# Performance work log

Hardware: AMD Instinct MI355X
Metric: run time of the kernel (lower is better)

The kernel has to match this reference:

```python
import jax, jax.numpy as jnp
import numpy as np

EPS = 1e-6  # torch.nn.PairwiseDistance default eps: dist = ||x - y + eps||_2


def setup_inputs() -> dict:
    key = jax.random.key(0)
    k1, k2 = jax.random.split(key)
    samples = jax.random.normal(k1, (4096, 128), dtype=jnp.float32)   # batch of observations
    V = jax.random.uniform(k2, (65536, 128), dtype=jnp.float32)       # grown node codebook (torch.rand init)
    return {"samples": samples, "V": V}


def reference(samples, V):
    # activate_bmu, vectorized over the batch.
    # torch PairwiseDistance(p=2): d_n = || x - V_n + eps ||_2
    D = samples.shape[-1]
    x_sq = jnp.sum(samples * samples, axis=-1)        # [B]
    v_sq = jnp.sum(V * V, axis=-1)                    # [N]
    xv = jnp.einsum('bd,nd->bn', samples, V)          # [B, N]
    x_sum = jnp.sum(samples, axis=-1)                 # [B]
    v_sum = jnp.sum(V, axis=-1)                       # [N]
    sq = (x_sq[:, None] + v_sq[None, :] - 2.0 * xv
          + 2.0 * EPS * (x_sum[:, None] - v_sum[None, :]) + D * EPS * EPS)
    dists = jnp.sqrt(jnp.maximum(sq, 0.0))            # [B, N]
    # top-2 smallest distances -> BMU b, second BMU s
    neg_top2, idx = jax.lax.top_k(-dists, 2)          # [B, 2]
    b = idx[:, 0]
    s = idx[:, 1]
    a = jnp.exp(neg_top2[:, 0])                       # exp(-b_dist)
    return (b, s, a)
```

## Files before the change

### kernel.cpp

```cpp
#include <hip/hip_runtime.h>
#include <math.h>

#define NS 4096
#define NV 65536
#define DDIM 128
#define EPSV 1e-6f
#define NCHUNK 16
#define TILES_PER_CHUNK 32
#define FLTMAX 3.402823466e+38f
#define IMAX 0x7fffffff

#define VSQ_F   0
#define VSUM_F  65536
#define XSQ_F   131072
#define XSUM_F  135168
#define PART_F  139264
#define WS_TILED_BYTE 1605632
#define TILE_BYTES 65536
#define TILE_STRIDE 66560

typedef __attribute__((ext_vector_type(8)))  __bf16        bf16x8;
typedef __attribute__((ext_vector_type(8)))  unsigned short ush8;
typedef __attribute__((ext_vector_type(4)))  unsigned short ush4;
typedef __attribute__((ext_vector_type(16))) float          f32x16;

typedef const __attribute__((address_space(1))) unsigned int* gp_t;
typedef __attribute__((address_space(3))) unsigned int*       lp_t;

__device__ __forceinline__ void async_cp16(const void* g, void* l) {
    __builtin_amdgcn_global_load_lds((gp_t)g, (lp_t)l, 16, 0, 0);
}

__device__ __forceinline__ unsigned short f2bf(float x) {
    unsigned u = __builtin_bit_cast(unsigned, x);
    u += 0x7FFFu + ((u >> 16) & 1u);
    return (unsigned short)(u >> 16);
}
__device__ __forceinline__ float bf2f(unsigned short h) {
    unsigned u = ((unsigned)h) << 16;
    return __builtin_bit_cast(float, u);
}

__device__ __forceinline__ void merge2t(float& d1, int& i1, float& d2, int& i2,
                                        float d, int i) {
    bool b1 = (d < d1) || (d == d1 && i < i1);
    bool b2 = (d < d2) || (d == d2 && i < i2);
    if (b1) { d2 = d1; i2 = i1; d1 = d; i1 = i; }
    else if (b2) { d2 = d; i2 = i; }
}

__global__ void vq_precompute(const float* __restrict__ samples,
                              const float* __restrict__ V,
                              float* __restrict__ ws) {
    const int wave = threadIdx.x >> 6;
    const int lane = threadIdx.x & 63;
    int row = blockIdx.x * 4 + wave;
    const float* src; float* sqo; float* sumo; int r;
    if (row < NV) {
        r = row; src = V + (size_t)r * DDIM; sqo = ws + VSQ_F; sumo = ws + VSUM_F;
    } else {
        r = row - NV;
        if (r >= NS) return;
        src = samples + (size_t)r * DDIM; sqo = ws + XSQ_F; sumo = ws + XSUM_F;
    }
    float2 v = ((const float2*)src)[lane];
    float s = v.x + v.y;
    float q = v.x * v.x + v.y * v.y;
    #pragma unroll
    for (int off = 32; off >= 1; off >>= 1) {
        s += __shfl_xor(s, off);
        q += __shfl_xor(q, off);
    }
    if (lane == 0) { sqo[r] = q; sumo[r] = s; }
}

__global__ void vq_cj(const float* __restrict__ ws_f, char* __restrict__ ws) {
    int c = blockIdx.x * 256 + threadIdx.x;
    float cj = ws_f[VSQ_F + c] - 2.0f * EPSV * ws_f[VSUM_F + c];
    int tile = c >> 7, m = c & 127;
    *(float*)(ws + WS_TILED_BYTE + (size_t)tile * TILE_STRIDE + TILE_BYTES + m * 4) = cj;
}

__global__ void vq_convertV(const float* __restrict__ V, char* __restrict__ ws) {
    const int tile = blockIdx.x;
    const int tid = threadIdx.x;
    char* dst = ws + WS_TILED_BYTE + (size_t)tile * TILE_STRIDE;
    const float4* v4 = (const float4*)V;
    #pragma unroll
    for (int i = 0; i < 16; i++) {
        int flat = i * 256 + tid;
        int row = flat >> 5;
        int kq  = flat & 31;
        float4 g = v4[(size_t)(tile * 128 + row) * 32 + kq];
        int k0 = kq * 4;
        int s = k0 >> 4, q = (k0 >> 3) & 1, j0 = k0 & 7;
        float xs[4] = {g.x, g.y, g.z, g.w};
        ush4 h, l;
        #pragma unroll
        for (int e = 0; e < 4; e++) {
            unsigned short hh = f2bf(xs[e]);
            h[e] = hh;
            l[e] = f2bf(xs[e] - bf2f(hh));
        }
        *(ush4*)(dst + ((((s * 2 + 0) * 2 + q) * 128) + row) * 16 + j0 * 2) = h;
        *(ush4*)(dst + ((((s * 2 + 1) * 2 + q) * 128) + row) * 16 + j0 * 2) = l;
    }
}

__global__ __launch_bounds__(256, 2)
void vq_gemm_topk(const float* __restrict__ samples, char* __restrict__ ws) {
    __shared__ __align__(16) char lds[TILE_STRIDE];
    const int tid = threadIdx.x;
    const int w = tid >> 6, lane = tid & 63;
    const int l31 = lane & 31, q = lane >> 5;
    const int st = blockIdx.x;
    const int chunk = blockIdx.y;
    const int nrow = st * 128 + w * 32 + l31;

    ush8 bh[8], bl[8];
    const float4* s4 = (const float4*)samples;
    #pragma unroll
    for (int s = 0; s < 8; s++) {
        float4 x0 = s4[(size_t)nrow * 32 + s * 4 + q * 2];
        float4 x1 = s4[(size_t)nrow * 32 + s * 4 + q * 2 + 1];
        float xs[8] = {x0.x, x0.y, x0.z, x0.w, x1.x, x1.y, x1.z, x1.w};
        #pragma unroll
        for (int j = 0; j < 8; j++) {
            float y = -2.0f * xs[j];
            unsigned short hh = f2bf(y);
            bh[s][j] = hh;
            bl[s][j] = f2bf(y - bf2f(hh));
        }
    }

    float d1 = FLTMAX, d2 = FLTMAX;
    int i1 = IMAX, i2 = IMAX;

    const char* tile0 = ws + WS_TILED_BYTE + (size_t)(chunk * TILES_PER_CHUNK) * TILE_STRIDE;

    for (int it = 0; it < TILES_PER_CHUNK; it++) {
        const char* src = tile0 + (size_t)it * TILE_STRIDE;
        #pragma unroll
        for (int i = 0; i < 16; i++) {
            int off = (i * 256 + tid) * 16;
            async_cp16(src + off, lds + off);
        }
        if (tid < 64) {
            int off = TILE_BYTES + tid * 16;
            async_cp16(src + off, lds + off);
        }
        __syncthreads();

        f32x16 acc[4];
        #pragma unroll
        for (int mi = 0; mi < 4; mi++)
            #pragma unroll
            for (int r = 0; r < 16; r++) acc[mi][r] = 0.0f;

        #pragma unroll
        for (int s = 0; s < 8; s++) {
            bf16x8 bhs = __builtin_bit_cast(bf16x8, bh[s]);
            bf16x8 bls = __builtin_bit_cast(bf16x8, bl[s]);
            #pragma unroll
            for (int mi = 0; mi < 4; mi++) {
                bf16x8 ah = *(const bf16x8*)(lds + (size_t)((((s * 2 + 0) * 2 + q) * 128) + mi * 32 + l31) * 16);
                bf16x8 al = *(const bf16x8*)(lds + (size_t)((((s * 2 + 1) * 2 + q) * 128) + mi * 32 + l31) * 16);
                acc[mi] = __builtin_amdgcn_mfma_f32_32x32x16_bf16(ah, bhs, acc[mi], 0, 0, 0);
                acc[mi] = __builtin_amdgcn_mfma_f32_32x32x16_bf16(ah, bls, acc[mi], 0, 0, 0);
                acc[mi] = __builtin_amdgcn_mfma_f32_32x32x16_bf16(al, bhs, acc[mi], 0, 0, 0);
            }
        }

        const int cbase = chunk * 4096 + it * 128 + 4 * q;
        #pragma unroll
        for (int mi = 0; mi < 4; mi++) {
            #pragma unroll
            for (int g = 0; g < 4; g++) {
                float4 cj = *(const float4*)(lds + TILE_BYTES + (size_t)(mi * 32 + g * 8 + 4 * q) * 4);
                float cje[4] = {cj.x, cj.y, cj.z, cj.w};
                #pragma unroll
                for (int e = 0; e < 4; e++) {
                    float v = acc[mi][g * 4 + e] + cje[e];
                    int idx = cbase + mi * 32 + g * 8 + e;
                    bool c1 = v < d1, c2 = v < d2;
                    float nd2 = c1 ? d1 : v;
                    int   ni2 = c1 ? i1 : idx;
                    d2 = c2 ? nd2 : d2;
                    i2 = c2 ? ni2 : i2;
                    d1 = c1 ? v : d1;
                    i1 = c1 ? idx : i1;
                }
            }
        }
        __syncthreads();
    }

    {
        float od1 = __shfl_xor(d1, 32), od2 = __shfl_xor(d2, 32);
        int   oi1 = __shfl_xor(i1, 32), oi2 = __shfl_xor(i2, 32);
        merge2t(d1, i1, d2, i2, od1, oi1);
        merge2t(d1, i1, d2, i2, od2, oi2);
    }
    if (q == 0) {
        int sample = st * 128 + w * 32 + l31;
        float4* part = (float4*)( (float*)((char*)ws) + PART_F );
        part[(size_t)sample * NCHUNK + chunk] = make_float4(d1, d2, (float)i1, (float)i2);
    }
}

__global__ void vq_reduce(const float* __restrict__ ws_f, float* __restrict__ out) {
    int m = blockIdx.x * 256 + threadIdx.x;
    if (m >= NS) return;
    const float4* part = (const float4*)(ws_f + PART_F);
    float d1 = FLTMAX, d2 = FLTMAX;
    int i1 = IMAX, i2 = IMAX;
    for (int c = 0; c < NCHUNK; c++) {
        float4 p = part[(size_t)m * NCHUNK + c];
        merge2t(d1, i1, d2, i2, p.x, (int)p.z);
        merge2t(d1, i1, d2, i2, p.y, (int)p.w);
    }
    float ci = ws_f[XSQ_F + m] + 2.0f * EPSV * ws_f[XSUM_F + m] + (float)DDIM * EPSV * EPSV;
    float sq = fmaxf(ci + d1, 0.0f);
    out[m]          = (float)i1;
    out[NS + m]     = (float)i2;
    out[2 * NS + m] = expf(-sqrtf(sq));
}

extern "C" void kernel_launch(void* const* d_in, const int* in_sizes, int n_in,
                              void* d_out, int out_size, void* d_ws, size_t ws_size,
                              hipStream_t stream) {
    (void)in_sizes; (void)n_in; (void)out_size; (void)ws_size;
    const float* samples = (const float*)d_in[0];
    const float* V = (const float*)d_in[1];
    float* out = (float*)d_out;
    float* ws_f = (float*)d_ws;
    char*  ws_b = (char*)d_ws;

    vq_precompute<<<dim3((NV + NS) / 4), 256, 0, stream>>>(samples, V, ws_f);
    vq_cj<<<dim3(NV / 256), 256, 0, stream>>>(ws_f, ws_b);
    vq_convertV<<<dim3(NV / 128), 256, 0, stream>>>(V, ws_b);
    vq_gemm_topk<<<dim3(NS / 128, NCHUNK), 256, 0, stream>>>(samples, ws_b);
    vq_reduce<<<dim3(NS / 256), 256, 0, stream>>>(ws_f, out);
}
```

Measured before the change: 299.1 us.

## Double-buffer codebook tiles, widen GEMM block to 512 threads, fuse cj precompute

Fuses the cj computation into the norm precompute kernel, which removes one launch. vq_convertV now writes 16-byte stores per row. The main GEMM kernel uses 512 threads, with each block covering 256 samples split across a 2x4 wave grid. Codebook tiles are double-buffered in LDS with async copies so the next tile loads while the current one is computed. The top-2 update is skipped via a wave ballot when no lane improves, and a final LDS merge combines the two wave rows. The cost is more LDS per block and more registers per wave, which may limit occupancy.

```diff
diff --git a/kernel.cpp b/kernel.cpp
--- a/kernel.cpp
+++ b/kernel.cpp
@@ -10,18 +10,16 @@
 #define FLTMAX 3.402823466e+38f
 #define IMAX 0x7fffffff
 
-#define VSQ_F   0
-#define VSUM_F  65536
 #define XSQ_F   131072
 #define XSUM_F  135168
 #define PART_F  139264
 #define WS_TILED_BYTE 1605632
 #define TILE_BYTES 65536
 #define TILE_STRIDE 66560
+#define BUFB 66560
 
 typedef __attribute__((ext_vector_type(8)))  __bf16        bf16x8;
 typedef __attribute__((ext_vector_type(8)))  unsigned short ush8;
-typedef __attribute__((ext_vector_type(4)))  unsigned short ush4;
 typedef __attribute__((ext_vector_type(16))) float          f32x16;
 
 typedef const __attribute__((address_space(1))) unsigned int* gp_t;
@@ -51,18 +49,15 @@
 
 __global__ void vq_precompute(const float* __restrict__ samples,
                               const float* __restrict__ V,
-                              float* __restrict__ ws) {
+                              float* __restrict__ ws_f, char* __restrict__ ws_b) {
     const int wave = threadIdx.x >> 6;
     const int lane = threadIdx.x & 63;
     int row = blockIdx.x * 4 + wave;
-    const float* src; float* sqo; float* sumo; int r;
-    if (row < NV) {
-        r = row; src = V + (size_t)r * DDIM; sqo = ws + VSQ_F; sumo = ws + VSUM_F;
-    } else {
-        r = row - NV;
-        if (r >= NS) return;
-        src = samples + (size_t)r * DDIM; sqo = ws + XSQ_F; sumo = ws + XSUM_F;
-    }
+    const float* src;
+    bool isV = (row < NV);
+    int r = isV ? row : row - NV;
+    if (!isV && r >= NS) return;
+    src = (isV ? V : samples) + (size_t)r * DDIM;
     float2 v = ((const float2*)src)[lane];
     float s = v.x + v.y;
     float q = v.x * v.x + v.y * v.y;
@@ -71,140 +66,179 @@
         s += __shfl_xor(s, off);
         q += __shfl_xor(q, off);
     }
-    if (lane == 0) { sqo[r] = q; sumo[r] = s; }
-}
-
-__global__ void vq_cj(const float* __restrict__ ws_f, char* __restrict__ ws) {
-    int c = blockIdx.x * 256 + threadIdx.x;
-    float cj = ws_f[VSQ_F + c] - 2.0f * EPSV * ws_f[VSUM_F + c];
-    int tile = c >> 7, m = c & 127;
-    *(float*)(ws + WS_TILED_BYTE + (size_t)tile * TILE_STRIDE + TILE_BYTES + m * 4) = cj;
+    if (lane == 0) {
+        if (isV) {
+            int tile = r >> 7, m = r & 127;
+            *(float*)(ws_b + WS_TILED_BYTE + (size_t)tile * TILE_STRIDE + TILE_BYTES + m * 4)
+                = q - 2.0f * EPSV * s;
+        } else {
+            ws_f[XSQ_F + r] = q;
+            ws_f[XSUM_F + r] = s;
+        }
+    }
 }
 
 __global__ void vq_convertV(const float* __restrict__ V, char* __restrict__ ws) {
     const int tile = blockIdx.x;
     const int tid = threadIdx.x;
+    const int q = tid >> 7, row = tid & 127;
     char* dst = ws + WS_TILED_BYTE + (size_t)tile * TILE_STRIDE;
-    const float4* v4 = (const float4*)V;
-    #pragma unroll
-    for (int i = 0; i < 16; i++) {
-        int flat = i * 256 + tid;
-        int row = flat >> 5;
-        int kq  = flat & 31;
-        float4 g = v4[(size_t)(tile * 128 + row) * 32 + kq];
-        int k0 = kq * 4;
-        int s = k0 >> 4, q = (k0 >> 3) & 1, j0 = k0 & 7;
-        float xs[4] = {g.x, g.y, g.z, g.w};
-        ush4 h, l;
-        #pragma unroll
-        for (int e = 0; e < 4; e++) {
+    const float4* v4 = (const float4*)(V + (size_t)(tile * 128 + row) * DDIM);
+    #pragma unroll
+    for (int s = 0; s < 8; s++) {
+        float4 g0 = v4[s * 4 + q * 2];
+        float4 g1 = v4[s * 4 + q * 2 + 1];
+        float xs[8] = {g0.x, g0.y, g0.z, g0.w, g1.x, g1.y, g1.z, g1.w};
+        ush8 h, l;
+        #pragma unroll
+        for (int e = 0; e < 8; e++) {
             unsigned short hh = f2bf(xs[e]);
             h[e] = hh;
             l[e] = f2bf(xs[e] - bf2f(hh));
         }
-        *(ush4*)(dst + ((((s * 2 + 0) * 2 + q) * 128) + row) * 16 + j0 * 2) = h;
-        *(ush4*)(dst + ((((s * 2 + 1) * 2 + q) * 128) + row) * 16 + j0 * 2) = l;
-    }
-}
-
-__global__ __launch_bounds__(256, 2)
+        *(ush8*)(dst + ((((s * 2 + 0) * 2 + q) * 128) + row) * 16) = h;
+        *(ush8*)(dst + ((((s * 2 + 1) * 2 + q) * 128) + row) * 16) = l;
+    }
+}
+
+__global__ __launch_bounds__(512, 2)
 void vq_gemm_topk(const float* __restrict__ samples, char* __restrict__ ws) {
-    __shared__ __align__(16) char lds[TILE_STRIDE];
+    __shared__ __align__(16) char lds[2 * BUFB];
     const int tid = threadIdx.x;
     const int w = tid >> 6, lane = tid & 63;
     const int l31 = lane & 31, q = lane >> 5;
+    const int wy = w >> 2, wx = w & 3;
     const int st = blockIdx.x;
     const int chunk = blockIdx.y;
-    const int nrow = st * 128 + w * 32 + l31;
-
-    ush8 bh[8], bl[8];
+
+    ush8 bh[2][8], bl[2][8];
     const float4* s4 = (const float4*)samples;
     #pragma unroll
-    for (int s = 0; s < 8; s++) {
-        float4 x0 = s4[(size_t)nrow * 32 + s * 4 + q * 2];
-        float4 x1 = s4[(size_t)nrow * 32 + s * 4 + q * 2 + 1];
-        float xs[8] = {x0.x, x0.y, x0.z, x0.w, x1.x, x1.y, x1.z, x1.w};
-        #pragma unroll
-        for (int j = 0; j < 8; j++) {
-            float y = -2.0f * xs[j];
-            unsigned short hh = f2bf(y);
-            bh[s][j] = hh;
-            bl[s][j] = f2bf(y - bf2f(hh));
-        }
-    }
-
-    float d1 = FLTMAX, d2 = FLTMAX;
-    int i1 = IMAX, i2 = IMAX;
+    for (int nb = 0; nb < 2; nb++) {
+        const int nrow = st * 256 + wx * 64 + nb * 32 + l31;
+        #pragma unroll
+        for (int s = 0; s < 8; s++) {
+            float4 x0 = s4[(size_t)nrow * 32 + s * 4 + q * 2];
+            float4 x1 = s4[(size_t)nrow * 32 + s * 4 + q * 2 + 1];
+            float xs[8] = {x0.x, x0.y, x0.z, x0.w, x1.x, x1.y, x1.z, x1.w};
+            #pragma unroll
+            for (int j = 0; j < 8; j++) {
+                float y = -2.0f * xs[j];
+                unsigned short hh = f2bf(y);
+                bh[nb][s][j] = hh;
+                bl[nb][s][j] = f2bf(y - bf2f(hh));
+            }
+        }
+    }
+
+    float d1[2] = {FLTMAX, FLTMAX}, d2[2] = {FLTMAX, FLTMAX};
+    int i1[2] = {IMAX, IMAX}, i2[2] = {IMAX, IMAX};
 
     const char* tile0 = ws + WS_TILED_BYTE + (size_t)(chunk * TILES_PER_CHUNK) * TILE_STRIDE;
 
+    auto stage = [&](int it) {
+        const char* src = tile0 + (size_t)it * TILE_STRIDE;
+        char* dstb = lds + (it & 1) * BUFB;
+        #pragma unroll
+        for (int i = 0; i < 8; i++) {
+            int off = (i * 512 + tid) * 16;
+            async_cp16(src + off, dstb + off);
+        }
+        if (tid < 32) {
+            int off = TILE_BYTES + tid * 16;
+            async_cp16(src + off, dstb + off);
+        }
+    };
+
+    stage(0);
+    __syncthreads();
+
     for (int it = 0; it < TILES_PER_CHUNK; it++) {
-        const char* src = tile0 + (size_t)it * TILE_STRIDE;
-        #pragma unroll
-        for (int i = 0; i < 16; i++) {
-            int off = (i * 256 + tid) * 16;
-            async_cp16(src + off, lds + off);
-        }
-        if (tid < 64) {
-            int off = TILE_BYTES + tid * 16;
-            async_cp16(src + off, lds + off);
-        }
-        __syncthreads();
+        if (it + 1 < TILES_PER_CHUNK) stage(it + 1);
+        const char* buf = lds + (it & 1) * BUFB;
 
         f32x16 acc[4];
         #pragma unroll
-        for (int mi = 0; mi < 4; mi++)
-            #pragma unroll
-            for (int r = 0; r < 16; r++) acc[mi][r] = 0.0f;
+        for (int a = 0; a < 4; a++)
+            #pragma unroll
+            for (int r = 0; r < 16; r++) acc[a][r] = 0.0f;
 
         #pragma unroll
         for (int s = 0; s < 8; s++) {
-            bf16x8 bhs = __builtin_bit_cast(bf16x8, bh[s]);
-            bf16x8 bls = __builtin_bit_cast(bf16x8, bl[s]);
-            #pragma unroll
-            for (int mi = 0; mi < 4; mi++) {
-                bf16x8 ah = *(const bf16x8*)(lds + (size_t)((((s * 2 + 0) * 2 + q) * 128) + mi * 32 + l31) * 16);
-                bf16x8 al = *(const bf16x8*)(lds + (size_t)((((s * 2 + 1) * 2 + q) * 128) + mi * 32 + l31) * 16);
-                acc[mi] = __builtin_amdgcn_mfma_f32_32x32x16_bf16(ah, bhs, acc[mi], 0, 0, 0);
-                acc[mi] = __builtin_amdgcn_mfma_f32_32x32x16_bf16(ah, bls, acc[mi], 0, 0, 0);
-                acc[mi] = __builtin_amdgcn_mfma_f32_32x32x16_bf16(al, bhs, acc[mi], 0, 0, 0);
+            #pragma unroll
+            for (int mi = 0; mi < 2; mi++) {
+                bf16x8 ah = *(const bf16x8*)(buf + (size_t)((((s * 2 + 0) * 2 + q) * 128) + wy * 64 + mi * 32 + l31) * 16);
+                bf16x8 al = *(const bf16x8*)(buf + (size_t)((((s * 2 + 1) * 2 + q) * 128) + wy * 64 + mi * 32 + l31) * 16);
+                #pragma unroll
+                for (int nb = 0; nb < 2; nb++) {
+                    bf16x8 bhs = __builtin_bit_cast(bf16x8, bh[nb][s]);
+                    bf16x8 bls = __builtin_bit_cast(bf16x8, bl[nb][s]);
+                    acc[mi * 2 + nb] = __builtin_amdgcn_mfma_f32_32x32x16_bf16(ah, bhs, acc[mi * 2 + nb], 0, 0, 0);
+                    acc[mi * 2 + nb] = __builtin_amdgcn_mfma_f32_32x32x16_bf16(ah, bls, acc[mi * 2 + nb], 0, 0, 0);
+                    acc[mi * 2 + nb] = __builtin_amdgcn_mfma_f32_32x32x16_bf16(al, bhs, acc[mi * 2 + nb], 0, 0, 0);
+                }
             }
         }
 
-        const int cbase = chunk * 4096 + it * 128 + 4 * q;
-        #pragma unroll
-        for (int mi = 0; mi < 4; mi++) {
+        const int ibase = chunk * 4096 + it * 128 + wy * 64 + 4 * q;
+        #pragma unroll
+        for (int mi = 0; mi < 2; mi++) {
             #pragma unroll
             for (int g = 0; g < 4; g++) {
-                float4 cj = *(const float4*)(lds + TILE_BYTES + (size_t)(mi * 32 + g * 8 + 4 * q) * 4);
+                float4 cj = *(const float4*)(buf + TILE_BYTES + (size_t)(wy * 64 + mi * 32 + g * 8 + 4 * q) * 4);
                 float cje[4] = {cj.x, cj.y, cj.z, cj.w};
                 #pragma unroll
-                for (int e = 0; e < 4; e++) {
-                    float v = acc[mi][g * 4 + e] + cje[e];
-                    int idx = cbase + mi * 32 + g * 8 + e;
-                    bool c1 = v < d1, c2 = v < d2;
-                    float nd2 = c1 ? d1 : v;
-                    int   ni2 = c1 ? i1 : idx;
-                    d2 = c2 ? nd2 : d2;
-                    i2 = c2 ? ni2 : i2;
-                    d1 = c1 ? v : d1;
-                    i1 = c1 ? idx : i1;
+                for (int nb = 0; nb < 2; nb++) {
+                    #pragma unroll
+                    for (int e = 0; e < 4; e++) {
+                        float v = acc[mi * 2 + nb][g * 4 + e] + cje[e];
+                        int idx = ibase + mi * 32 + g * 8 + e;
+                        if (__builtin_expect(__ballot(v < d2[nb]) != 0, 0)) {
+                            bool c1 = v < d1[nb];
+                            float t2 = c1 ? d1[nb] : v;
+                            int   j2 = c1 ? i1[nb] : idx;
+                            bool c2 = v < d2[nb];
+                            d2[nb] = c2 ? t2 : d2[nb];
+                            i2[nb] = c2 ? j2 : i2[nb];
+                            d1[nb] = c1 ? v  : d1[nb];
+                            i1[nb] = c1 ? idx : i1[nb];
+                        }
+                    }
                 }
             }
         }
         __syncthreads();
     }
 
-    {
-        float od1 = __shfl_xor(d1, 32), od2 = __shfl_xor(d2, 32);
-        int   oi1 = __shfl_xor(i1, 32), oi2 = __shfl_xor(i2, 32);
-        merge2t(d1, i1, d2, i2, od1, oi1);
-        merge2t(d1, i1, d2, i2, od2, oi2);
-    }
-    if (q == 0) {
-        int sample = st * 128 + w * 32 + l31;
-        float4* part = (float4*)( (float*)((char*)ws) + PART_F );
-        part[(size_t)sample * NCHUNK + chunk] = make_float4(d1, d2, (float)i1, (float)i2);
+    #pragma unroll
+    for (int nb = 0; nb < 2; nb++) {
+        float od1 = __shfl_xor(d1[nb], 32), od2 = __shfl_xor(d2[nb], 32);
+        int   oi1 = __shfl_xor(i1[nb], 32), oi2 = __shfl_xor(i2[nb], 32);
+        merge2t(d1[nb], i1[nb], d2[nb], i2[nb], od1, oi1);
+        merge2t(d1[nb], i1[nb], d2[nb], i2[nb], od2, oi2);
+    }
+
+    float4* mscratch = (float4*)lds;
+    if (wy == 1 && q == 0) {
+        #pragma unroll
+        for (int nb = 0; nb < 2; nb++) {
+            int sl = wx * 64 + nb * 32 + l31;
+            mscratch[sl] = make_float4(d1[nb], d2[nb], (float)i1[nb], (float)i2[nb]);
+        }
+    }
+    __syncthreads();
+    if (wy == 0 && q == 0) {
+        float4* part = (float4*)((float*)ws + PART_F);
+        #pragma unroll
+        for (int nb = 0; nb < 2; nb++) {
+            int sl = wx * 64 + nb * 32 + l31;
+            float4 o = mscratch[sl];
+            merge2t(d1[nb], i1[nb], d2[nb], i2[nb], o.x, (int)o.z);
+            merge2t(d1[nb], i1[nb], d2[nb], i2[nb], o.y, (int)o.w);
+            int sample = st * 256 + sl;
+            part[(size_t)sample * NCHUNK + chunk] =
+                make_float4(d1[nb], d2[nb], (float)i1[nb], (float)i2[nb]);
+        }
     }
 }
 
@@ -236,9 +270,8 @@
     float* ws_f = (float*)d_ws;
     char*  ws_b = (char*)d_ws;
 
-    vq_precompute<<<dim3((NV + NS) / 4), 256, 0, stream>>>(samples, V, ws_f);
-    vq_cj<<<dim3(NV / 256), 256, 0, stream>>>(ws_f, ws_b);
+    vq_precompute<<<dim3((NV + NS) / 4), 256, 0, stream>>>(samples, V, ws_f, ws_b);
     vq_convertV<<<dim3(NV / 128), 256, 0, stream>>>(V, ws_b);
-    vq_gemm_topk<<<dim3(NS / 128, NCHUNK), 256, 0, stream>>>(samples, ws_b);
+    vq_gemm_topk<<<dim3(NS / 256, NCHUNK), 512, 0, stream>>>(samples, ws_b);
     vq_reduce<<<dim3(NS / 256), 256, 0, stream>>>(ws_f, out);
 }
```

Result: slower. 389.7 us (+30.3%).
